# Kernel optimization log

Hardware: AMD Instinct MI355X
Metric: run time of the kernel (lower is better)

## Reference

```python
import jax, jax.numpy as jnp
import numpy as np

# Mamba2 hyperparams fixed by MambaBlock.__init__ (d_model=512, d_state=128, d_conv=4, expand=4, headdim=64)
D_MODEL = 512
D_STATE = 128      # N
D_CONV = 4
EXPAND = 4
HEADDIM = 64       # P
D_INNER = EXPAND * D_MODEL            # 2048
NHEADS = D_INNER // HEADDIM           # 32
NGROUPS = 1
CONV_DIM = D_INNER + 2 * NGROUPS * D_STATE      # 2304 (x, B, C share the depthwise conv)
D_IN_PROJ = 2 * D_INNER + 2 * NGROUPS * D_STATE + NHEADS  # 4384 (z, xBC, dt)
EPS = 1e-5


def _mamba2(x, in_w, conv_w, conv_b, dt_bias, A_log, Dp, norm_w, out_w):
    """Faithful Mamba2 forward (ngroups=1). x: [B, L, d_model]."""
    Bsz, L, _ = x.shape
    zxbcdt = jnp.einsum('bld,pd->blp', x, in_w)  # in_proj (no bias)
    z, xBC, dt = jnp.split(zxbcdt, [D_INNER, D_INNER + CONV_DIM], axis=-1)
    # causal depthwise conv1d over xBC, kernel size D_CONV, then SiLU
    xp = jnp.pad(xBC, ((0, 0), (D_CONV - 1, 0), (0, 0)))
    xBC = sum(xp[:, k:k + L, :] * conv_w[:, k] for k in range(D_CONV)) + conv_b
    xBC = jax.nn.silu(xBC)
    xs, Bc, Cc = jnp.split(xBC, [D_INNER, D_INNER + D_STATE], axis=-1)
    xs = xs.reshape(Bsz, L, NHEADS, HEADDIM)          # [B,L,H,P]
    dt = jax.nn.softplus(dt + dt_bias)                 # [B,L,H]
    A = -jnp.exp(A_log)                                # [H]
    dA = jnp.exp(dt * A)                               # [B,L,H] discrete state decay

    def step(h, inp):
        dA_t, dt_t, x_t, B_t, C_t = inp  # [B,H],[B,H],[B,H,P],[B,N],[B,N]
        h = h * dA_t[:, :, None, None] + (dt_t[:, :, None] * x_t)[..., None] * B_t[:, None, None, :]
        y = jnp.einsum('bhpn,bn->bhp', h, C_t)
        return h, y

    h0 = jnp.zeros((Bsz, NHEADS, HEADDIM, D_STATE), x.dtype)
    inps = (dA.transpose(1, 0, 2), dt.transpose(1, 0, 2), xs.transpose(1, 0, 2, 3),
            Bc.transpose(1, 0, 2), Cc.transpose(1, 0, 2))
    _, ys = jax.lax.scan(step, h0, inps)               # [L,B,H,P]
    y = ys.transpose(1, 0, 2, 3) + Dp[None, None, :, None] * xs  # skip via D
    y = y.reshape(Bsz, L, D_INNER)
    # RMSNormGated (norm_before_gate=False): gate first, then RMSNorm
    y = y * jax.nn.silu(z)
    y = y * jax.lax.rsqrt(jnp.mean(y * y, axis=-1, keepdims=True) + EPS) * norm_w
    return jnp.einsum('bld,od->blo', y, out_w)         # out_proj (no bias)


def _make_params(key):
    ks = jax.random.split(key, 8)
    return dict(
        in_w=jax.random.normal(ks[0], (D_IN_PROJ, D_MODEL), jnp.float32) / np.sqrt(D_MODEL),
        conv_w=jax.random.normal(ks[1], (CONV_DIM, D_CONV), jnp.float32) * 0.2,
        conv_b=jax.random.normal(ks[2], (CONV_DIM,), jnp.float32) * 0.02,
        dt_bias=jax.random.normal(ks[3], (NHEADS,), jnp.float32) * 0.1,
        A_log=jnp.log(jax.random.uniform(ks[4], (NHEADS,), jnp.float32, 1.0, 16.0)),
        D=jnp.ones((NHEADS,), jnp.float32),
        norm_w=jnp.ones((D_INNER,), jnp.float32),
        out_w=jax.random.normal(ks[5], (D_MODEL, D_INNER), jnp.float32) / np.sqrt(D_INNER),
    )


def setup_inputs() -> dict:
    key = jax.random.key(0)
    k_in, k_f, k_b = jax.random.split(key, 3)
    x = jax.random.normal(k_in, (2, 2048, D_MODEL), jnp.float32)
    pf = _make_params(k_f)
    pb = _make_params(k_b)
    out = {'input': x}
    for n, v in pf.items():
        out['f_' + n] = v
    for n, v in pb.items():
        out['b_' + n] = v
    return out


def reference(input, f_in_w, f_conv_w, f_conv_b, f_dt_bias, f_A_log, f_D, f_norm_w, f_out_w,
              b_in_w, b_conv_w, b_conv_b, b_dt_bias, b_A_log, b_D, b_norm_w, b_out_w):
    fwd = _mamba2(input, f_in_w, f_conv_w, f_conv_b, f_dt_bias, f_A_log, f_D, f_norm_w, f_out_w)
    xb = jnp.flip(input, axis=1)
    bwd = _mamba2(xb, b_in_w, b_conv_w, b_conv_b, b_dt_bias, b_A_log, b_D, b_norm_w, b_out_w)
    bwd = jnp.flip(bwd, axis=1)
    return jnp.concatenate([fwd + input, bwd + input], axis=-1)
```

## Files before the change

### kernel.cpp

```cpp
#include <hip/hip_runtime.h>
#include <hip/hip_bf16.h>
#include <math.h>

#define L_SEQ   2048
#define M_ROWS  4096
#define DPROJ   4384
#define DPROJP  4480
#define NPROJ   4352
#define DINNER  2048
#define CONVDIM 2304
#define NST     128
#define NH      32
#define CHUNK   128
#define NCH     16
#define CTR     32
#define NTILE   (L_SEQ / CTR)
#define LOG2E   1.4426950408889634f

typedef __attribute__((ext_vector_type(8))) short short8;
typedef __attribute__((ext_vector_type(4))) float f32x4;
typedef unsigned short u16;

static __device__ __forceinline__ u16 bf16bits(float v) {
    __hip_bfloat16 t = __float2bfloat16(v);
    return *(u16*)&t;
}
static __device__ __forceinline__ float bits2f(u16 u) {
    return __uint_as_float((unsigned)u << 16);
}
static __device__ __forceinline__ int sidx(int row, int s) {
    return (row << 7) + ((((s >> 3) ^ (row & 7)) << 3) | (s & 7));
}
static __device__ __forceinline__ int sslot(int row, int ks) {
    return (row << 7) + ((ks ^ (row & 7)) << 3);
}
static __device__ __forceinline__ void gload16(const void* g, void* l) {
    __builtin_amdgcn_global_load_lds(
        (const __attribute__((address_space(1))) void*)g,
        (__attribute__((address_space(3))) void*)l, 16, 0, 0);
}

__global__ __launch_bounds__(256) void cvt_x_kernel(
    const float* __restrict__ x, u16* __restrict__ xbf)
{
    const int i = (blockIdx.x * 256 + threadIdx.x) * 4;
    const float4 v = *(const float4*)(x + i);
    xbf[i + 0] = bf16bits(v.x);
    xbf[i + 1] = bf16bits(v.y);
    xbf[i + 2] = bf16bits(v.z);
    xbf[i + 3] = bf16bits(v.w);
}

__global__ __launch_bounds__(256) void cvt_win_kernel(
    const float* __restrict__ w0, const float* __restrict__ w1,
    u16* __restrict__ dst)
{
    const int dir = blockIdx.y;
    const float* __restrict__ w = dir ? w1 : w0;
    u16* __restrict__ d = dst + (size_t)dir * NPROJ * 512;
    const int i = (blockIdx.x * 256 + threadIdx.x) * 4;
    const float4 v = *(const float4*)(w + i);
    d[i + 0] = bf16bits(v.x);
    d[i + 1] = bf16bits(v.y);
    d[i + 2] = bf16bits(v.z);
    d[i + 3] = bf16bits(v.w);
}

__global__ __launch_bounds__(256) void cvt_wout_kernel(
    const float* __restrict__ w0, const float* __restrict__ w1,
    u16* __restrict__ dst)
{
    const int dir = blockIdx.y;
    const float* __restrict__ w = dir ? w1 : w0;
    u16* __restrict__ d = dst + (size_t)dir * 512 * DINNER;
    const int i = (blockIdx.x * 256 + threadIdx.x) * 4;
    const float4 v = *(const float4*)(w + i);
    d[i + 0] = bf16bits(v.x);
    d[i + 1] = bf16bits(v.y);
    d[i + 2] = bf16bits(v.z);
    d[i + 3] = bf16bits(v.w);
}

__global__ __launch_bounds__(256) void gemm_mfma_in(
    const u16* __restrict__ A0, int lda,
    const u16* __restrict__ Bw, long long b_dir_off,
    u16* __restrict__ Cb, long long c_dir_off, int ldc,
    int K)
{
    const int dir = blockIdx.z;
    const int nwg  = gridDim.x * gridDim.y;
    const int flat = blockIdx.y * gridDim.x + blockIdx.x;
    const int q = nwg >> 3, r = nwg & 7;
    const int xcd = flat & 7, idx = flat >> 3;
    const int wg = (xcd < r) ? xcd * (q + 1) + idx
                             : r * (q + 1) + (xcd - r) * q + idx;
    const int m0 = (wg / gridDim.x) * 128;
    const int n0 = (wg % gridDim.x) * 128;

    const u16* __restrict__ A = A0;
    const u16* __restrict__ B = Bw + (size_t)dir * b_dir_off;

    __shared__ u16 Asl[128 * 64];
    __shared__ u16 Bsl[128 * 64];

    const int tid  = threadIdx.x;
    const int lane = tid & 63;
    const int wid  = tid >> 6;
    const int wr   = (wid >> 1) << 6;
    const int wc   = (wid & 1) << 6;
    const int l15  = lane & 15;
    const int l4   = lane >> 4;

    f32x4 acc[4][4];
#pragma unroll
    for (int m = 0; m < 4; ++m)
#pragma unroll
        for (int n = 0; n < 4; ++n) acc[m][n] = (f32x4)0.f;

    for (int k0 = 0; k0 < K; k0 += 64) {
        __syncthreads();
#pragma unroll
        for (int i = 0; i < 4; ++i) {
            const int c    = tid + (i << 8);
            const int row  = c >> 3;
            const int scol = ((c & 7) ^ (row & 7)) << 3;
            gload16(A + (size_t)(m0 + row) * lda + k0 + scol, (char*)Asl + (c << 4));
            gload16(B + (size_t)(n0 + row) * K   + k0 + scol, (char*)Bsl + (c << 4));
        }
        __syncthreads();

#pragma unroll
        for (int kh = 0; kh < 2; ++kh) {
            const int ks = (kh << 2) + l4;
            short8 a[4], b[4];
#pragma unroll
            for (int m = 0; m < 4; ++m) {
                const int R = wr + (m << 4) + l15;
                a[m] = *(const short8*)((const char*)Asl + (R << 7) + ((ks ^ (R & 7)) << 4));
            }
#pragma unroll
            for (int n = 0; n < 4; ++n) {
                const int R = wc + (n << 4) + l15;
                b[n] = *(const short8*)((const char*)Bsl + (R << 7) + ((ks ^ (R & 7)) << 4));
            }
#pragma unroll
            for (int m = 0; m < 4; ++m)
#pragma unroll
                for (int n = 0; n < 4; ++n)
                    acc[m][n] = __builtin_amdgcn_mfma_f32_16x16x32_bf16(
                        a[m], b[n], acc[m][n], 0, 0, 0);
        }
    }

#pragma unroll
    for (int m = 0; m < 4; ++m) {
        const int row0 = m0 + wr + (m << 4) + (l4 << 2);
#pragma unroll
        for (int n = 0; n < 4; ++n) {
            const int col = n0 + wc + (n << 4) + l15;
#pragma unroll
            for (int r2 = 0; r2 < 4; ++r2)
                Cb[(size_t)dir * c_dir_off + (size_t)(row0 + r2) * ldc + col] =
                    bf16bits(acc[m][n][r2]);
        }
    }
}

__global__ __launch_bounds__(256) void gemm_out_kernel(
    const u16* __restrict__ Azx,
    const u16* __restrict__ Bw,
    const float* __restrict__ x,
    float* __restrict__ out)
{
    const int dir = blockIdx.z;
    const int nwg  = gridDim.x * gridDim.y;
    const int flat = blockIdx.y * gridDim.x + blockIdx.x;
    const int q = nwg >> 3;
    const int xcd = flat & 7, idx = flat >> 3;
    const int wg = xcd * q + idx;
    const int m0 = (wg >> 3) * 128;
    const int n0 = (wg & 7) * 64;

    const u16* __restrict__ A = Azx + (size_t)dir * M_ROWS * DPROJP + DINNER;
    const u16* __restrict__ B = Bw + (size_t)dir * 512 * DINNER;

    __shared__ u16 Asl[128 * 64];
    __shared__ u16 Bsl[64 * 64];

    const int tid  = threadIdx.x;
    const int lane = tid & 63;
    const int wid  = tid >> 6;
    const int wr   = (wid >> 1) << 6;
    const int wc   = (wid & 1) << 5;
    const int l15  = lane & 15;
    const int l4   = lane >> 4;

    f32x4 acc[4][2];
#pragma unroll
    for (int m = 0; m < 4; ++m)
#pragma unroll
        for (int n = 0; n < 2; ++n) acc[m][n] = (f32x4)0.f;

    for (int k0 = 0; k0 < DINNER; k0 += 64) {
        __syncthreads();
#pragma unroll
        for (int i = 0; i < 4; ++i) {
            const int c    = tid + (i << 8);
            const int row  = c >> 3;
            const int scol = ((c & 7) ^ (row & 7)) << 3;
            gload16(A + (size_t)(m0 + row) * DPROJP + k0 + scol, (char*)Asl + (c << 4));
        }
#pragma unroll
        for (int i = 0; i < 2; ++i) {
            const int c    = tid + (i << 8);
            const int row  = c >> 3;
            const int scol = ((c & 7) ^ (row & 7)) << 3;
            gload16(B + (size_t)(n0 + row) * DINNER + k0 + scol, (char*)Bsl + (c << 4));
        }
        __syncthreads();

#pragma unroll
        for (int kh = 0; kh < 2; ++kh) {
            const int ks = (kh << 2) + l4;
            short8 a[4], b[2];
#pragma unroll
            for (int m = 0; m < 4; ++m) {
                const int R = wr + (m << 4) + l15;
                a[m] = *(const short8*)((const char*)Asl + (R << 7) + ((ks ^ (R & 7)) << 4));
            }
#pragma unroll
            for (int n = 0; n < 2; ++n) {
                const int R = wc + (n << 4) + l15;
                b[n] = *(const short8*)((const char*)Bsl + (R << 7) + ((ks ^ (R & 7)) << 4));
            }
#pragma unroll
            for (int m = 0; m < 4; ++m)
#pragma unroll
                for (int n = 0; n < 2; ++n)
                    acc[m][n] = __builtin_amdgcn_mfma_f32_16x16x32_bf16(
                        a[m], b[n], acc[m][n], 0, 0, 0);
        }
    }

#pragma unroll
    for (int m = 0; m < 4; ++m) {
        const int row0 = m0 + wr + (m << 4) + (l4 << 2);
#pragma unroll
        for (int n = 0; n < 2; ++n) {
            const int col = n0 + wc + (n << 4) + l15;
#pragma unroll
            for (int r2 = 0; r2 < 4; ++r2) {
                const float v = acc[m][n][r2] + x[(size_t)(row0 + r2) * 512 + col];
                out[(size_t)(row0 + r2) * 1024 + dir * 512 + col] = v;
            }
        }
    }
}

__global__ __launch_bounds__(256) void conv_kernel(
    const u16* __restrict__ zx,
    const float* __restrict__ cw0, const float* __restrict__ cw1,
    const float* __restrict__ cb0, const float* __restrict__ cb1,
    u16* __restrict__ xs, u16* __restrict__ Bbf, u16* __restrict__ Cbf)
{
    const int dir = blockIdx.z;
    const int c   = blockIdx.x * 256 + threadIdx.x;
    const int b   = blockIdx.y >> 6;
    const int r0  = (blockIdx.y & (NTILE - 1)) * CTR;

    const float* __restrict__ cw = dir ? cw1 : cw0;
    const float w0 = cw[c * 4 + 0], w1 = cw[c * 4 + 1];
    const float w2 = cw[c * 4 + 2], w3 = cw[c * 4 + 3];
    const float bias = (dir ? cb1 : cb0)[c];

    const u16* __restrict__ zcol = zx + (size_t)dir * M_ROWS * DPROJP
        + (size_t)(b * L_SEQ) * DPROJP + DINNER + c;
    const size_t obase = (size_t)(dir * M_ROWS + b * L_SEQ);

    auto emit = [&](int l, float acc) {
        const float s = acc / (1.f + expf(-acc));
        const size_t orow = obase + l;
        if (c < DINNER)            xs[orow * DINNER + c] = bf16bits(s);
        else if (c < DINNER + NST) Bbf[orow * NST + (c - DINNER)] = bf16bits(s);
        else                       Cbf[orow * NST + (c - DINNER - NST)] = bf16bits(s);
    };

    if (dir == 0) {
        float h0 = (r0 - 3 >= 0) ? bits2f(zcol[(size_t)(r0 - 3) * DPROJP]) : 0.f;
        float h1 = (r0 - 2 >= 0) ? bits2f(zcol[(size_t)(r0 - 2) * DPROJP]) : 0.f;
        float h2 = (r0 - 1 >= 0) ? bits2f(zcol[(size_t)(r0 - 1) * DPROJP]) : 0.f;
#pragma unroll 8
        for (int l = r0; l < r0 + CTR; ++l) {
            const float zl = bits2f(zcol[(size_t)l * DPROJP]);
            float acc = bias;
            acc = fmaf(w0, h0, acc);
            acc = fmaf(w1, h1, acc);
            acc = fmaf(w2, h2, acc);
            acc = fmaf(w3, zl, acc);
            emit(l, acc);
            h0 = h1; h1 = h2; h2 = zl;
        }
    } else {
        const int le = r0 + CTR - 1;
        float h1 = (le + 1 < L_SEQ) ? bits2f(zcol[(size_t)(le + 1) * DPROJP]) : 0.f;
        float h2 = (le + 2 < L_SEQ) ? bits2f(zcol[(size_t)(le + 2) * DPROJP]) : 0.f;
        float h3 = (le + 3 < L_SEQ) ? bits2f(zcol[(size_t)(le + 3) * DPROJP]) : 0.f;
#pragma unroll 8
        for (int l = le; l >= r0; --l) {
            const float zl = bits2f(zcol[(size_t)l * DPROJP]);
            float acc = bias;
            acc = fmaf(w3, zl, acc);
            acc = fmaf(w2, h1, acc);
            acc = fmaf(w1, h2, acc);
            acc = fmaf(w0, h3, acc);
            emit(l, acc);
            h3 = h2; h2 = h1; h1 = zl;
        }
    }
}

__global__ __launch_bounds__(512) void dt_kernel(
    const float* __restrict__ x,
    const float* __restrict__ inw0, const float* __restrict__ inw1,
    const float* __restrict__ dtbias0, const float* __restrict__ dtbias1,
    const float* __restrict__ Alog0, const float* __restrict__ Alog1,
    float* __restrict__ dtb, float* __restrict__ dta)
{
    const int dir = blockIdx.y;
    const int r0  = blockIdx.x * 64;
    const int tid = threadIdx.x;

    __shared__ float wT[512 * 32];
    __shared__ float sbias[NH], sa[NH];

    const float* __restrict__ w = (dir ? inw1 : inw0) + (size_t)(DINNER + CONVDIM) * 512;
    for (int i = tid; i < 4096; i += 512) {
        const int flat = i * 4;
        const int h = flat >> 9;
        const int k = flat & 511;
        const float4 v = *(const float4*)(w + flat);
        *(float4*)&wT[(k >> 2) * 128 + h * 4] = v;
    }
    if (tid < NH) {
        sbias[tid] = (dir ? dtbias1 : dtbias0)[tid];
        sa[tid] = -expf((dir ? Alog1 : Alog0)[tid]) * LOG2E;
    }
    __syncthreads();

    const int h  = tid & 31;
    const int rr = tid >> 5;
    const float bias = sbias[h];
    const float a = sa[h];

    for (int rp = 0; rp < 64; rp += 16) {
        const int row = r0 + rp + rr;
        const float4* __restrict__ xr = (const float4*)(x + (size_t)row * 512);
        float4 s4 = make_float4(0.f, 0.f, 0.f, 0.f);
#pragma unroll 8
        for (int k4 = 0; k4 < 128; ++k4) {
            const float4 xv = xr[k4];
            const float4 wv = *(const float4*)&wT[k4 * 128 + h * 4];
            s4.x = fmaf(xv.x, wv.x, s4.x);
            s4.y = fmaf(xv.y, wv.y, s4.y);
            s4.z = fmaf(xv.z, wv.z, s4.z);
            s4.w = fmaf(xv.w, wv.w, s4.w);
        }
        const float v = (s4.x + s4.y) + (s4.z + s4.w) + bias;
        const float sp = (v > 20.f) ? v : log1pf(expf(v));
        const size_t orow = (size_t)(dir * M_ROWS + row);
        dtb[orow * NH + h] = sp;
        dta[orow * NH + h] = sp * a;
    }
}

__global__ __launch_bounds__(256) void sraw_kernel(
    const u16* __restrict__ Bbf, const u16* __restrict__ Cbf,
    u16* __restrict__ Sraw)
{
    const int bx  = blockIdx.x;
    const int ch  = bx & (NCH - 1);
    const int db  = bx >> 4;
    const int dir = db >> 1, bb = db & 1;
    const int tid = threadIdx.x;
    const int wid = tid >> 6;
    const int lane = tid & 63;
    const int l15 = lane & 15, l4 = lane >> 4;
    const int t0  = ch * CHUNK;
    const size_t dbase = (size_t)(dir * M_ROWS + bb * L_SEQ);
    const size_t base  = ((size_t)bx) << 14;

    auto lidx = [&](int t) { return dir ? (L_SEQ - 1 - t) : t; };

    f32x4 accs[2][8];
#pragma unroll
    for (int m = 0; m < 2; ++m)
#pragma unroll
        for (int j = 0; j < 8; ++j) accs[m][j] = (f32x4)0.f;

    short8 af[2][4];
#pragma unroll
    for (int m = 0; m < 2; ++m) {
        const size_t crow = dbase + lidx(t0 + wid * 32 + m * 16 + l15);
#pragma unroll
        for (int kk = 0; kk < 4; ++kk)
            af[m][kk] = *(const short8*)(Cbf + crow * NST + kk * 32 + l4 * 8);
    }
#pragma unroll
    for (int j = 0; j < 8; ++j) {
        const size_t brow = dbase + lidx(t0 + j * 16 + l15);
        short8 bf_[4];
#pragma unroll
        for (int kk = 0; kk < 4; ++kk)
            bf_[kk] = *(const short8*)(Bbf + brow * NST + kk * 32 + l4 * 8);
#pragma unroll
        for (int m = 0; m < 2; ++m)
#pragma unroll
            for (int kk = 0; kk < 4; ++kk)
                accs[m][j] = __builtin_amdgcn_mfma_f32_16x16x32_bf16(
                    af[m][kk], bf_[kk], accs[m][j], 0, 0, 0);
    }

#pragma unroll
    for (int m = 0; m < 2; ++m)
#pragma unroll
        for (int j = 0; j < 8; ++j)
#pragma unroll
            for (int r = 0; r < 4; ++r) {
                const int t = wid * 32 + m * 16 + l4 * 4 + r;
                const int s = j * 16 + l15;
                Sraw[base + (size_t)t * 128 + s] = bf16bits(accs[m][j][r]);
            }
}

__global__ __launch_bounds__(256) void ssd_state_kernel(
    const u16* __restrict__ xs, const u16* __restrict__ Bbf,
    const float* __restrict__ dtb, const float* __restrict__ dta,
    u16* __restrict__ stateC, float* __restrict__ betac)
{
    const int bx  = blockIdx.x;
    const int ch  = bx & (NCH - 1);
    const int bh  = bx >> 4;
    const int dir = bh >> 6;
    const int bb  = (bh >> 5) & 1;
    const int h   = bh & 31;
    const int tid = threadIdx.x;
    const int wid = tid >> 6;
    const int lane = tid & 63;
    const int l15 = lane & 15;
    const int l4  = lane >> 4;
    const int t0  = ch * CHUNK;
    const size_t dbase = (size_t)(dir * M_ROWS + bb * L_SEQ);

    __shared__ u16 XT[64 * 128];
    __shared__ u16 WBT[64 * 128];
    __shared__ float scum[CHUNK];
    __shared__ float sdt[CHUNK];

    auto lidx = [&](int t) { return dir ? (L_SEQ - 1 - t) : t; };

    if (tid >= 128) {
        const int s = tid - 128;
        sdt[s] = dtb[(dbase + lidx(t0 + s)) * NH + h];
    }
    if (wid == 0) {
        float a0 = dta[(dbase + lidx(t0 + lane)) * NH + h];
        float a1 = dta[(dbase + lidx(t0 + 64 + lane)) * NH + h];
#pragma unroll
        for (int off = 1; off < 64; off <<= 1) {
            const float u0 = __shfl_up(a0, off);
            const float u1 = __shfl_up(a1, off);
            if (lane >= off) { a0 += u0; a1 += u1; }
        }
        a1 += __shfl(a0, 63);
        scum[lane] = a0; scum[64 + lane] = a1;
        betac[(size_t)bh * L_SEQ + t0 + lane] = a0;
        betac[(size_t)bh * L_SEQ + t0 + 64 + lane] = a1;
    }
    __syncthreads();

    {
        const int s = tid >> 1;
        const float dts = sdt[s];
        const size_t grow = dbase + lidx(t0 + s);
        const int p0 = (tid & 1) * 32;
        const u16* __restrict__ xp = xs + grow * DINNER + h * 64 + p0;
#pragma unroll
        for (int q = 0; q < 4; ++q) {
            short8 v = *(const short8*)(xp + q * 8);
#pragma unroll
            for (int j = 0; j < 8; ++j) {
                const int p = p0 + q * 8 + j;
                XT[sidx(p, s)] = bf16bits(dts * bits2f((u16)v[j]));
            }
        }
    }

    const size_t sbase = ((size_t)bh * NCH + ch) * 8192;

#pragma unroll
    for (int half = 0; half < 2; ++half) {
        const int noff = half * 64;
        {
            const int s = tid >> 1;
            const float rs = exp2f(scum[CHUNK - 1] - scum[s]);
            const size_t grow = dbase + lidx(t0 + s);
            const int n0l = (tid & 1) * 32;
            const u16* __restrict__ bp = Bbf + grow * NST + noff + n0l;
#pragma unroll
            for (int q = 0; q < 4; ++q) {
                short8 v = *(const short8*)(bp + q * 8);
#pragma unroll
                for (int j = 0; j < 8; ++j) {
                    const int nl = n0l + q * 8 + j;
                    WBT[sidx(nl, s)] = bf16bits(rs * bits2f((u16)v[j]));
                }
            }
        }
        __syncthreads();

        {
            const int pw = wid * 16;
            const int prow = pw + l15;
            short8 xa[4];
#pragma unroll
            for (int kk = 0; kk < 4; ++kk)
                xa[kk] = *(const short8*)(XT + sslot(prow, kk * 4 + l4));
#pragma unroll
            for (int jn = 0; jn < 4; ++jn) {
                const int nl = jn * 16 + l15;
                f32x4 acc = (f32x4)0.f;
#pragma unroll
                for (int kk = 0; kk < 4; ++kk) {
                    const short8 wb = *(const short8*)(WBT + sslot(nl, kk * 4 + l4));
                    acc = __builtin_amdgcn_mfma_f32_16x16x32_bf16(xa[kk], wb, acc, 0, 0, 0);
                }
#pragma unroll
                for (int r = 0; r < 4; ++r)
                    stateC[sbase + (size_t)(pw + l4 * 4 + r) * 128 + noff + jn * 16 + l15] =
                        bf16bits(acc[r]);
            }
        }
        __syncthreads();
    }
}

__global__ __launch_bounds__(512) void combine_kernel(
    u16* __restrict__ stateC, const float* __restrict__ betac)
{
    const int bh  = blockIdx.x;
    const int tid = threadIdx.x;

    float hrun[16];
#pragma unroll
    for (int j = 0; j < 16; ++j) hrun[j] = 0.f;

    for (int s = 0; s < NCH; ++s) {
        const size_t off = ((size_t)bh * NCH + s) * 8192 + (size_t)tid * 16;
        float c[16];
#pragma unroll
        for (int j = 0; j < 16; ++j) c[j] = bits2f(stateC[off + j]);
#pragma unroll
        for (int j = 0; j < 16; ++j) stateC[off + j] = bf16bits(hrun[j]);
        const float alpha = exp2f(betac[(size_t)bh * L_SEQ + s * CHUNK + (CHUNK - 1)]);
#pragma unroll
        for (int j = 0; j < 16; ++j) hrun[j] = fmaf(alpha, hrun[j], c[j]);
    }
}

__global__ __launch_bounds__(512) void ssd_out_kernel(
    const u16* __restrict__ xs, const u16* __restrict__ Cbf,
    const u16* __restrict__ Sraw, const u16* __restrict__ stateC,
    const float* __restrict__ dtb, const float* __restrict__ betac,
    const float* __restrict__ D0, const float* __restrict__ D1,
    u16* __restrict__ yb)
{
    const int bx  = blockIdx.x;
    const int ch  = bx & (NCH - 1);
    const int bh  = bx >> 4;
    const int dir = bh >> 6;
    const int bb  = (bh >> 5) & 1;
    const int h   = bh & 31;
    const int tid = threadIdx.x;
    const int wid = tid >> 6;
    const int lane = tid & 63;
    const int l15 = lane & 15;
    const int l4  = lane >> 4;
    const int t0  = ch * CHUNK;
    const size_t dbase = (size_t)(dir * M_ROWS + bb * L_SEQ);
    const float Dv = (dir ? D1 : D0)[h];

    __shared__ u16 XT[64 * 128];
    __shared__ u16 HS[64 * 128];
    __shared__ float scum[CHUNK];
    __shared__ float sdt[CHUNK];

    auto lidx = [&](int t) { return dir ? (L_SEQ - 1 - t) : t; };

    const int trow = wid * 16 + l15;
    const size_t sbraw = ((size_t)(((bh >> 5) * NCH) + ch)) << 14;
    const size_t crow = dbase + lidx(t0 + trow);
    const size_t sbase = ((size_t)bh * NCH + ch) * 8192;

    short8 sv[4], c8[4];
#pragma unroll
    for (int kk = 0; kk < 4; ++kk) {
        const int sb = kk * 32 + l4 * 8;
        sv[kk] = *(const short8*)(Sraw + sbraw + (size_t)trow * 128 + sb);
        c8[kk] = *(const short8*)(Cbf + crow * NST + sb);
    }
    u16 xsv[16];
#pragma unroll
    for (int jp = 0; jp < 4; ++jp)
#pragma unroll
        for (int r = 0; r < 4; ++r) {
            const int t = wid * 16 + l4 * 4 + r;
            xsv[jp * 4 + r] =
                xs[(dbase + lidx(t0 + t)) * DINNER + h * 64 + jp * 16 + l15];
        }

#pragma unroll
    for (int i = 0; i < 2; ++i) {
        const int c = tid + (i << 9);
        const int row = c >> 4;
        const int sl  = c & 15;
        *(short8*)(HS + sslot(row, sl)) =
            *(const short8*)(stateC + sbase + (size_t)row * 128 + sl * 8);
    }
    if (tid < 128) {
        scum[tid] = betac[(size_t)bh * L_SEQ + t0 + tid];
    } else if (tid < 256) {
        const int s = tid - 128;
        sdt[s] = dtb[(dbase + lidx(t0 + s)) * NH + h];
    }
    __syncthreads();

    {
        const int s = tid >> 2;
        const float dts = sdt[s];
        const size_t grow = dbase + lidx(t0 + s);
        const int p0 = (tid & 3) * 16;
        const u16* __restrict__ xp = xs + grow * DINNER + h * 64 + p0;
#pragma unroll
        for (int q = 0; q < 2; ++q) {
            short8 v = *(const short8*)(xp + q * 8);
#pragma unroll
            for (int j = 0; j < 8; ++j) {
                const int p = p0 + q * 8 + j;
                XT[sidx(p, s)] = bf16bits(dts * bits2f((u16)v[j]));
            }
        }
    }
    __syncthreads();

    u16* __restrict__ ybase = yb + (size_t)dir * M_ROWS * DINNER;

    const float ct = scum[trow];
    const float gs = exp2f(ct);
    short8 pa[4], ga[4];
#pragma unroll
    for (int kk = 0; kk < 4; ++kk) {
        const int sb = kk * 32 + l4 * 8;
        short8 o, og;
#pragma unroll
        for (int j = 0; j < 8; ++j) {
            const float g = ((sb + j) <= trow) ? exp2f(ct - scum[sb + j]) : 0.f;
            o[j]  = (short)bf16bits(bits2f((u16)sv[kk][j]) * g);
            og[j] = (short)bf16bits(bits2f((u16)c8[kk][j]) * gs);
        }
        pa[kk] = o;
        ga[kk] = og;
    }

#pragma unroll
    for (int jp = 0; jp < 4; ++jp) {
        const int prow = jp * 16 + l15;
        short8 xb[4], hb[4];
#pragma unroll
        for (int kk = 0; kk < 4; ++kk) {
            xb[kk] = *(const short8*)(XT + sslot(prow, kk * 4 + l4));
            hb[kk] = *(const short8*)(HS + sslot(prow, kk * 4 + l4));
        }
        f32x4 acc = (f32x4)0.f;
#pragma unroll
        for (int kk = 0; kk < 4; ++kk)
            acc = __builtin_amdgcn_mfma_f32_16x16x32_bf16(
                pa[kk], xb[kk], acc, 0, 0, 0);
#pragma unroll
        for (int kk = 0; kk < 4; ++kk)
            acc = __builtin_amdgcn_mfma_f32_16x16x32_bf16(
                ga[kk], hb[kk], acc, 0, 0, 0);
#pragma unroll
        for (int r = 0; r < 4; ++r) {
            const int t = wid * 16 + l4 * 4 + r;
            const int lg = lidx(t0 + t);
            const float xv = bits2f(xsv[jp * 4 + r]);
            ybase[(size_t)(bb * L_SEQ + lg) * DINNER + h * 64 + prow] =
                bf16bits(acc[r] + Dv * xv);
        }
    }
}

__global__ __launch_bounds__(256) void gatenorm_kernel(
    u16* __restrict__ zx, const u16* __restrict__ yb,
    const float* __restrict__ nw0, const float* __restrict__ nw1)
{
    const int dir = blockIdx.y;
    const int row = blockIdx.x;
    const float* __restrict__ nw = dir ? nw1 : nw0;
    u16* __restrict__ zrow = zx + (size_t)dir * M_ROWS * DPROJP + (size_t)row * DPROJP;
    const u16* __restrict__ yrow = yb + (size_t)dir * M_ROWS * DINNER + (size_t)row * DINNER;
    const int tid = threadIdx.x;
    const int c0 = tid * 8;

    const short8 zv = *(const short8*)(zrow + c0);
    const short8 yv8 = *(const short8*)(yrow + c0);

    float g[8];
#pragma unroll
    for (int j = 0; j < 8; ++j) {
        const float z = bits2f((u16)zv[j]);
        g[j] = bits2f((u16)yv8[j]) * (z / (1.f + expf(-z)));
    }

    float ss = 0.f;
#pragma unroll
    for (int j = 0; j < 8; ++j) ss = fmaf(g[j], g[j], ss);
#pragma unroll
    for (int off = 1; off < 64; off <<= 1) ss += __shfl_xor(ss, off);
    __shared__ float red[4];
    if ((tid & 63) == 0) red[tid >> 6] = ss;
    __syncthreads();
    const float total = red[0] + red[1] + red[2] + red[3];
    const float rs = rsqrtf(total * (1.f / (float)DINNER) + 1e-5f);

    const float4 w0 = *(const float4*)(nw + c0);
    const float4 w1 = *(const float4*)(nw + c0 + 4);
    const float wv[8] = {w0.x, w0.y, w0.z, w0.w, w1.x, w1.y, w1.z, w1.w};
    short8 outv;
#pragma unroll
    for (int j = 0; j < 8; ++j) outv[j] = (short)bf16bits(g[j] * rs * wv[j]);
    *(short8*)(zrow + DINNER + c0) = outv;
}

extern "C" void kernel_launch(void* const* d_in, const int* in_sizes, int n_in,
                              void* d_out, int out_size, void* d_ws, size_t ws_size,
                              hipStream_t stream)
{
    (void)in_sizes; (void)n_in; (void)out_size; (void)ws_size;
    const float* x        = (const float*)d_in[0];
    const float* f_in_w   = (const float*)d_in[1];
    const float* f_conv_w = (const float*)d_in[2];
    const float* f_conv_b = (const float*)d_in[3];
    const float* f_dtbias = (const float*)d_in[4];
    const float* f_Alog   = (const float*)d_in[5];
    const float* f_D      = (const float*)d_in[6];
    const float* f_nw     = (const float*)d_in[7];
    const float* f_out_w  = (const float*)d_in[8];
    const float* b_in_w   = (const float*)d_in[9];
    const float* b_conv_w = (const float*)d_in[10];
    const float* b_conv_b = (const float*)d_in[11];
    const float* b_dtbias = (const float*)d_in[12];
    const float* b_Alog   = (const float*)d_in[13];
    const float* b_D      = (const float*)d_in[14];
    const float* b_nw     = (const float*)d_in[15];
    const float* b_out_w  = (const float*)d_in[16];

    u16* zx  = (u16*)d_ws;
    u16* xs  = zx + (size_t)2 * M_ROWS * DPROJP;
    u16* Bbf = xs + (size_t)2 * M_ROWS * DINNER;
    u16* Cbf = Bbf + (size_t)2 * M_ROWS * NST;
    float* dtb = (float*)(Cbf + (size_t)2 * M_ROWS * NST);
    float* dta = dtb + (size_t)2 * M_ROWS * NH;
    u16* stateC = (u16*)(dta + (size_t)2 * M_ROWS * NH);
    float* betac = (float*)(stateC + (size_t)128 * NCH * 8192);
    u16* yb = (u16*)(betac + (size_t)128 * L_SEQ);
    u16* x_bf   = yb + (size_t)2 * M_ROWS * DINNER;
    u16* w_in_bf  = x_bf + (size_t)M_ROWS * 512;
    u16* w_out_bf = w_in_bf + (size_t)2 * DPROJP * 512;
    u16* Sraw = w_out_bf + (size_t)2 * 512 * DINNER;

    cvt_x_kernel<<<dim3(M_ROWS * 512 / 1024), 256, 0, stream>>>(x, x_bf);
    cvt_win_kernel<<<dim3(NPROJ * 512 / 1024, 2), 256, 0, stream>>>(f_in_w, b_in_w, w_in_bf);
    cvt_wout_kernel<<<dim3(512 * DINNER / 1024, 2), 256, 0, stream>>>(f_out_w, b_out_w, w_out_bf);

    gemm_mfma_in<<<dim3(NPROJ / 128, M_ROWS / 128, 2), 256, 0, stream>>>(
        x_bf, 512,
        w_in_bf, (long long)NPROJ * 512,
        zx, (long long)M_ROWS * DPROJP, DPROJP,
        512);

    conv_kernel<<<dim3(CONVDIM / 256, 2 * NTILE, 2), 256, 0, stream>>>(
        zx, f_conv_w, b_conv_w, f_conv_b, b_conv_b, xs, Bbf, Cbf);

    dt_kernel<<<dim3(M_ROWS / 64, 2), 512, 0, stream>>>(
        x, f_in_w, b_in_w, f_dtbias, b_dtbias, f_Alog, b_Alog, dtb, dta);

    sraw_kernel<<<dim3(4 * NCH), 256, 0, stream>>>(Bbf, Cbf, Sraw);

    ssd_state_kernel<<<dim3(128 * NCH), 256, 0, stream>>>(
        xs, Bbf, dtb, dta, stateC, betac);

    combine_kernel<<<dim3(128), 512, 0, stream>>>(stateC, betac);

    ssd_out_kernel<<<dim3(128 * NCH), 512, 0, stream>>>(
        xs, Cbf, Sraw, stateC, dtb, betac, f_D, b_D, yb);

    gatenorm_kernel<<<dim3(M_ROWS, 2), 256, 0, stream>>>(zx, yb, f_nw, b_nw);

    gemm_out_kernel<<<dim3(8, 32, 2), 256, 0, stream>>>(
        zx, w_out_bf, x, (float*)d_out);
}
```

Measured before the change: 260.5 us.

## Restructure SSD state kernel to 512 threads with single-pass full-N staging

The chunk-state kernel now runs 512 threads per block and stages all 128 state columns of B into shared memory in one pass, where before it made two half passes with separate barriers. Global loads of x and B are issued into registers before the cumsum/dt setup, so their latency overlaps that work, and each wave handles a 16x64 output tile. This removes one load/compute round and two barriers per block, in exchange for twice the WBT shared memory and more threads per block, which may reduce how many blocks fit on a CU.

```diff
diff --git a/kernel.cpp b/kernel.cpp
--- a/kernel.cpp
+++ b/kernel.cpp
@@ -432,7 +432,7 @@
             }
 }
 
-__global__ __launch_bounds__(256) void ssd_state_kernel(
+__global__ __launch_bounds__(512) void ssd_state_kernel(
     const u16* __restrict__ xs, const u16* __restrict__ Bbf,
     const float* __restrict__ dtb, const float* __restrict__ dta,
     u16* __restrict__ stateC, float* __restrict__ betac)
@@ -452,13 +452,25 @@
     const size_t dbase = (size_t)(dir * M_ROWS + bb * L_SEQ);
 
     __shared__ u16 XT[64 * 128];
-    __shared__ u16 WBT[64 * 128];
+    __shared__ u16 WBT[128 * 128];
     __shared__ float scum[CHUNK];
     __shared__ float sdt[CHUNK];
 
     auto lidx = [&](int t) { return dir ? (L_SEQ - 1 - t) : t; };
 
-    if (tid >= 128) {
+    const int sP = tid >> 2;
+    const size_t grow = dbase + lidx(t0 + sP);
+    const int p0 = (tid & 3) * 16;
+    const int n0 = (tid & 3) * 32;
+    short8 xv[2], bv[4];
+#pragma unroll
+    for (int q = 0; q < 2; ++q)
+        xv[q] = *(const short8*)(xs + grow * DINNER + h * 64 + p0 + q * 8);
+#pragma unroll
+    for (int q = 0; q < 4; ++q)
+        bv[q] = *(const short8*)(Bbf + grow * NST + n0 + q * 8);
+
+    if (tid >= 128 && tid < 256) {
         const int s = tid - 128;
         sdt[s] = dtb[(dbase + lidx(t0 + s)) * NH + h];
     }
@@ -479,68 +491,42 @@
     __syncthreads();
 
     {
-        const int s = tid >> 1;
-        const float dts = sdt[s];
-        const size_t grow = dbase + lidx(t0 + s);
-        const int p0 = (tid & 1) * 32;
-        const u16* __restrict__ xp = xs + grow * DINNER + h * 64 + p0;
-#pragma unroll
-        for (int q = 0; q < 4; ++q) {
-            short8 v = *(const short8*)(xp + q * 8);
-#pragma unroll
-            for (int j = 0; j < 8; ++j) {
-                const int p = p0 + q * 8 + j;
-                XT[sidx(p, s)] = bf16bits(dts * bits2f((u16)v[j]));
-            }
-        }
-    }
-
+        const float dts = sdt[sP];
+        const float rs  = exp2f(scum[CHUNK - 1] - scum[sP]);
+#pragma unroll
+        for (int q = 0; q < 2; ++q)
+#pragma unroll
+            for (int j = 0; j < 8; ++j)
+                XT[sidx(p0 + q * 8 + j, sP)] = bf16bits(dts * bits2f((u16)xv[q][j]));
+#pragma unroll
+        for (int q = 0; q < 4; ++q)
+#pragma unroll
+            for (int j = 0; j < 8; ++j)
+                WBT[sidx(n0 + q * 8 + j, sP)] = bf16bits(rs * bits2f((u16)bv[q][j]));
+    }
+    __syncthreads();
+
+    const int pw = (wid >> 1) << 4;
+    const int nh = (wid & 1) << 6;
+    const int prow = pw + l15;
+    short8 xa[4];
+#pragma unroll
+    for (int kk = 0; kk < 4; ++kk)
+        xa[kk] = *(const short8*)(XT + sslot(prow, kk * 4 + l4));
     const size_t sbase = ((size_t)bh * NCH + ch) * 8192;
-
-#pragma unroll
-    for (int half = 0; half < 2; ++half) {
-        const int noff = half * 64;
-        {
-            const int s = tid >> 1;
-            const float rs = exp2f(scum[CHUNK - 1] - scum[s]);
-            const size_t grow = dbase + lidx(t0 + s);
-            const int n0l = (tid & 1) * 32;
-            const u16* __restrict__ bp = Bbf + grow * NST + noff + n0l;
-#pragma unroll
-            for (int q = 0; q < 4; ++q) {
-                short8 v = *(const short8*)(bp + q * 8);
-#pragma unroll
-                for (int j = 0; j < 8; ++j) {
-                    const int nl = n0l + q * 8 + j;
-                    WBT[sidx(nl, s)] = bf16bits(rs * bits2f((u16)v[j]));
-                }
-            }
-        }
-        __syncthreads();
-
-        {
-            const int pw = wid * 16;
-            const int prow = pw + l15;
-            short8 xa[4];
-#pragma unroll
-            for (int kk = 0; kk < 4; ++kk)
-                xa[kk] = *(const short8*)(XT + sslot(prow, kk * 4 + l4));
-#pragma unroll
-            for (int jn = 0; jn < 4; ++jn) {
-                const int nl = jn * 16 + l15;
-                f32x4 acc = (f32x4)0.f;
-#pragma unroll
-                for (int kk = 0; kk < 4; ++kk) {
-                    const short8 wb = *(const short8*)(WBT + sslot(nl, kk * 4 + l4));
-                    acc = __builtin_amdgcn_mfma_f32_16x16x32_bf16(xa[kk], wb, acc, 0, 0, 0);
-                }
-#pragma unroll
-                for (int r = 0; r < 4; ++r)
-                    stateC[sbase + (size_t)(pw + l4 * 4 + r) * 128 + noff + jn * 16 + l15] =
-                        bf16bits(acc[r]);
-            }
-        }
-        __syncthreads();
+#pragma unroll
+    for (int jn = 0; jn < 4; ++jn) {
+        const int nrow = nh + jn * 16 + l15;
+        f32x4 acc = (f32x4)0.f;
+#pragma unroll
+        for (int kk = 0; kk < 4; ++kk) {
+            const short8 wb = *(const short8*)(WBT + sslot(nrow, kk * 4 + l4));
+            acc = __builtin_amdgcn_mfma_f32_16x16x32_bf16(xa[kk], wb, acc, 0, 0, 0);
+        }
+#pragma unroll
+        for (int r = 0; r < 4; ++r)
+            stateC[sbase + (size_t)(pw + l4 * 4 + r) * 128 + nh + jn * 16 + l15] =
+                bf16bits(acc[r]);
     }
 }
 
@@ -797,7 +783,7 @@
 
     sraw_kernel<<<dim3(4 * NCH), 256, 0, stream>>>(Bbf, Cbf, Sraw);
 
-    ssd_state_kernel<<<dim3(128 * NCH), 256, 0, stream>>>(
+    ssd_state_kernel<<<dim3(128 * NCH), 512, 0, stream>>>(
         xs, Bbf, dtb, dta, stateC, betac);
 
     combine_kernel<<<dim3(128), 512, 0, stream>>>(stateC, betac);
```

Measured after the change: 263.9 us. No clear change (+1.3%).
